# Performance work log

Measured on AMD Instinct MI355X. Metric: run time of the kernel, lower is better.

Reference implementation:

```python
import jax, jax.numpy as jnp
import numpy as np

SLOPE = 0.01  # LeakyReLU default negative slope
EPS = 1e-5    # BatchNorm eps


def _lrelu(x):
    return jnp.where(x >= 0, x, SLOPE * x)


def _conv(x, w, b):
    # x: [B,C,H,W], w: [O,I,kh,kw] (torch layout)
    y = jax.lax.conv_general_dilated(x, w, (1, 1), 'VALID',
                                     dimension_numbers=('NCHW', 'OIHW', 'NCHW'))
    return y + b[None, :, None, None]


def _bn4(x, p):
    # eval-mode BatchNorm2d; p = [gamma, beta, running_mean, running_var] stacked [4,C]
    g, b, m, v = p
    s = g * jax.lax.rsqrt(v + EPS)
    return x * s[None, :, None, None] + (b - m * s)[None, :, None, None]


def _forward(observation, action, sc1_w, sc1_b, sbn1, sc2_w, sc2_b, sbn2,
             mc1_w, mc1_b, mbn1, mc2_w, mc2_b, mbn2,
             gw_root, gw_rel, g_b, gbn,
             a_cw, a_cb, a_w1, a_b1, a_w2, a_b2, a_w3, a_b3,
             edge_index, edge_type, nodes_to_select):
    # ---- multi-scale temporal CNN (eval mode: dropout = identity) ----
    s = _lrelu(_bn4(_conv(observation, sc1_w, sc1_b), sbn1))
    s = _lrelu(_bn4(_conv(s, sc2_w, sc2_b), sbn2))          # [B,20,N,1]
    m = _lrelu(_bn4(_conv(observation, mc1_w, mc1_b), mbn1))
    m = _lrelu(_bn4(_conv(m, mc2_w, mc2_b), mbn2))          # [B,20,N,1]
    l = _lrelu(jnp.max(observation, axis=3, keepdims=True)) # [B,3,N,1]
    temporal = jnp.concatenate([s, m, l], axis=1)           # [B,43,N,1]

    # ---- RGCN (graph replicated per batch element; aggr='mean' per relation) ----
    x = jnp.swapaxes(temporal[..., 0], 1, 2)                # [B,N,F]
    N = x.shape[1]
    src, dst = edge_index[0], edge_index[1]
    out = jnp.einsum('bnf,fg->bng', x, gw_root) + g_b       # root transform + bias
    for r in range(gw_rel.shape[0]):
        h = jnp.einsum('bnf,fg->bng', x, gw_rel[r])         # per-relation transform
        mask = (edge_type == r).astype(x.dtype)             # [E]
        msgs = h[:, src, :] * mask[None, :, None]           # [B,E,F] gather
        agg = jax.ops.segment_sum(jnp.swapaxes(msgs, 0, 1), dst, num_segments=N)  # [N,B,F]
        deg = jax.ops.segment_sum(mask, dst, num_segments=N)                       # [N]
        out = out + jnp.swapaxes(agg, 0, 1) / jnp.maximum(deg, 1.0)[None, :, None]
    # BatchNorm1d (eval) + LeakyReLU; dropout = identity
    g, be, mu, v = gbn
    sg = g * jax.lax.rsqrt(v + EPS)
    out = _lrelu(out * sg + (be - mu * sg))                 # [B,N,F]

    graph_feats = jnp.swapaxes(out, 1, 2)[..., None]        # [B,F,N,1]
    feats = jnp.concatenate([temporal, graph_feats], axis=1)  # [B,86,N,1]
    feats = feats[:, :, nodes_to_select, :]                 # [B,86,P,1]

    # ---- actor head (mode == 'actor'); cash_bias is zeroed in the original ----
    stocks = action[:, 1:][:, None, :, None]                # [B,1,P,1]
    f = jnp.concatenate([stocks, feats], axis=1)[..., 0]    # [B,87,P]
    logits = jnp.einsum('bcp,c->bp', f, a_cw) + a_cb[0]     # 1x1 conv, out_ch=1
    o = jnp.concatenate([jnp.zeros((f.shape[0], 1), f.dtype), logits], axis=1)  # [B,P+1]
    h1 = jax.nn.relu(o @ a_w1 + a_b1)
    h2 = jax.nn.relu(h1 @ a_w2 + a_b2)
    return jax.nn.softmax(h2 @ a_w3 + a_b3, axis=-1)


def setup_inputs() -> dict:
    key = jax.random.key(0)
    ks = jax.random.split(key, 30)
    B, C0, N, T = 64, 3, 500, 50
    E, R, P, H = 16000, 4, 500, 128
    CM, CF = 3, 20
    F = 2 * CF + C0  # 43

    def rn(k, sh, s=0.1):
        return jax.random.normal(k, sh, jnp.float32) * s

    def bn_p(k, c):
        k1, k2, k3, k4 = jax.random.split(k, 4)
        return jnp.stack([jax.random.uniform(k1, (c,), jnp.float32, 0.5, 1.5),
                          rn(k2, (c,)), rn(k3, (c,)),
                          jax.random.uniform(k4, (c,), jnp.float32, 0.5, 1.5)])

    return {
        'observation': jax.random.normal(ks[0], (B, C0, N, T), jnp.float32),
        'action': jax.random.uniform(ks[1], (B, P + 1), jnp.float32),
        'edge_index': jax.random.randint(ks[2], (2, E), 0, N),
        'edge_type': jax.random.randint(ks[3], (E,), 0, R),
        'nodes_to_select': jnp.arange(P),
        'sc1_w': rn(ks[4], (CM, C0, 1, 3)), 'sc1_b': rn(ks[5], (CM,)), 'sbn1': bn_p(ks[6], CM),
        'sc2_w': rn(ks[7], (CF, CM, 1, 48)), 'sc2_b': rn(ks[8], (CF,)), 'sbn2': bn_p(ks[9], CF),
        'mc1_w': rn(ks[10], (CM, C0, 1, 21)), 'mc1_b': rn(ks[11], (CM,)), 'mbn1': bn_p(ks[12], CM),
        'mc2_w': rn(ks[13], (CF, CM, 1, 30)), 'mc2_b': rn(ks[14], (CF,)), 'mbn2': bn_p(ks[15], CF),
        'gw_root': rn(ks[16], (F, F)), 'gw_rel': rn(ks[17], (R, F, F)),
        'g_b': rn(ks[18], (F,)), 'gbn': bn_p(ks[19], F),
        'a_cw': rn(ks[20], (2 * F + 1,)), 'a_cb': rn(ks[21], (1,)),
        'a_w1': rn(ks[22], (P + 1, H)), 'a_b1': rn(ks[23], (H,)),
        'a_w2': rn(ks[24], (H, H)), 'a_b2': rn(ks[25], (H,)),
        'a_w3': rn(ks[26], (H, P + 1)), 'a_b3': rn(ks[27], (P + 1,)),
    }


def reference(observation, action, edge_index, edge_type, nodes_to_select,
              sc1_w, sc1_b, sbn1, sc2_w, sc2_b, sbn2,
              mc1_w, mc1_b, mbn1, mc2_w, mc2_b, mbn2,
              gw_root, gw_rel, g_b, gbn,
              a_cw, a_cb, a_w1, a_b1, a_w2, a_b2, a_w3, a_b3):
    return _forward(observation, action, sc1_w, sc1_b, sbn1, sc2_w, sc2_b, sbn2,
                    mc1_w, mc1_b, mbn1, mc2_w, mc2_b, mbn2,
                    gw_root, gw_rel, g_b, gbn,
                    a_cw, a_cb, a_w1, a_b1, a_w2, a_b2, a_w3, a_b3,
                    edge_index, edge_type, nodes_to_select)
```

## Files before the change

### kernel.cpp

```cpp
#include <hip/hip_runtime.h>

#define SLOPE 0.01f
#define EPSV  1e-5f
#define BB    64
#define NN    500
#define TT    50
#define E_N   16000
#define FF    43
#define PP    500
#define HH    128
#define XSTRIDE 48
#define PAD_E 40

typedef const float* fp;

__device__ __forceinline__ float lrelu(float x){ return x >= 0.f ? x : SLOPE * x; }
__device__ __forceinline__ float bnap(float x, fp bnp, int c, int C){
  float g  = bnp[c], b_ = bnp[C + c];
  float m  = bnp[2*C + c], v = bnp[3*C + c];
  float s = g * rsqrtf(v + EPSV);
  return x * s + (b_ - m * s);
}

__global__ __launch_bounds__(1024) void k_prep16(
    fp sc2w, fp mc2w, fp gwroot, fp gwrel,
    float* __restrict__ wT_s2, float* __restrict__ wT_m2, float* __restrict__ wTg,
    float* __restrict__ o_ws,
    const int* __restrict__ ei, const int* __restrict__ et,
    int* __restrict__ cntg, int* __restrict__ esp)
{
  int tid = threadIdx.x, blk = blockIdx.x;
  if (blk == 0){
    for (int i = tid; i < 2880; i += 1024){ int o = i/144, x = i%144; wT_s2[x*20+o] = sc2w[i]; }
  } else if (blk == 1){
    for (int i = tid; i < 1800; i += 1024){ int o = i/90,  x = i%90;  wT_m2[x*20+o] = mc2w[i]; }
  } else if (blk < 6){
    for (int i = (blk-2)*1024 + tid; i < 9245; i += 4096){
      int f5 = i/43, g = i%43;
      wTg[i] = (f5 < 43) ? gwroot[f5*43+g] : gwrel[(f5-43)*43+g];
    }
  } else if (blk == 6){
    if (tid < BB) o_ws[tid*(PP+1)] = 0.f;
  } else if (blk == 7){
    for (int i = 9245 + tid; i < 9312; i += 1024) wTg[i] = 0.f;
  } else {
    int e = (blk - 8)*1024 + tid;
    if (e < E_N){
      int s = ei[e], d = ei[E_N + e], r = et[e];
      int idx = d*4 + r;
      int pos = atomicAdd(&cntg[idx], 1);
      if (pos < PAD_E) esp[idx*PAD_E + pos] = s;
    }
  }
}

__global__ __launch_bounds__(512, 2) void k_tempo16(
    fp obs,
    fp sc1w, fp sc1b, fp sbn1, fp sc2b, fp sbn2,
    fp mc1w, fp mc1b, fp mbn1, fp mc2b, fp mbn2,
    const float* __restrict__ wT_s2, const float* __restrict__ wT_m2,
    float* __restrict__ xbuf)
{
  __shared__ float smem[11776];
  #define OL(n,j)   smem[(n)*151 + (j)]
  #define PB(w,n,o) smem[(w)*1472 + (n)*23 + (o)]
  int tid = threadIdx.x;

  int w = __builtin_amdgcn_readfirstlane(tid >> 6);
  int lane = tid & 63;
  int b  = blockIdx.x >> 3;
  int n0 = (blockIdx.x & 7) << 6;
  int span = (NN - n0 < 64) ? (NN - n0) : 64;

  for (int c = 0; c < 3; c++){
    const float* base = obs + (size_t)(b*3 + c)*25000;
    for (int idx = tid; idx < 3200; idx += 512){
      int n = idx / 50, t = idx % 50;
      int node = n0 + n; if (node > NN-1) node = NN-1;
      OL(n, c*50 + t) = base[node*50 + t];
    }
  }
  __syncthreads();

  float acc[20];
  float mx[3] = {-1e30f, -1e30f, -1e30f};
  if (w < 5){
    int t0 = w * 6;
    float ov[3][26];
    #pragma unroll
    for (int ci = 0; ci < 3; ci++)
      #pragma unroll
      for (int j = 0; j < 26; j++)
        ov[ci][j] = OL(lane, ci*50 + t0 + j);
    float sc1[3], sh1[3];
    #pragma unroll
    for (int ci = 0; ci < 3; ci++){
      float s = mbn1[ci] * rsqrtf(mbn1[9+ci] + EPSV);
      sc1[ci] = s; sh1[ci] = mbn1[3+ci] - mbn1[6+ci]*s;
    }
    #pragma unroll
    for (int o = 0; o < 20; o++) acc[o] = 0.f;
    #pragma unroll
    for (int i = 0; i < 6; i++){
      int tt = t0 + i;
      float mv[3];
      #pragma unroll
      for (int co = 0; co < 3; co++) mv[co] = mc1b[co];
      #pragma unroll
      for (int ci = 0; ci < 3; ci++)
        #pragma unroll
        for (int k = 0; k < 21; k++){
          float v = ov[ci][i + k];
          #pragma unroll
          for (int co = 0; co < 3; co++) mv[co] += v * mc1w[co*63 + ci*21 + k];
        }
      #pragma unroll
      for (int co = 0; co < 3; co++){
        float z = lrelu(mv[co]*sc1[co] + sh1[co]);
        const float* wp = wT_m2 + (co*30 + tt)*20;
        #pragma unroll
        for (int o = 0; o < 20; o++) acc[o] += z * wp[o];
      }
    }
  } else {
    int ws_ = w - 5;
    int t0 = ws_ * 16;
    float ovs[3][18];
    #pragma unroll
    for (int ci = 0; ci < 3; ci++)
      #pragma unroll
      for (int j = 0; j < 18; j++)
        ovs[ci][j] = OL(lane, ci*50 + t0 + j);
    int l0 = ws_ * 17;
    int ln = (50 - l0 < 17) ? (50 - l0) : 17;
    for (int j = 0; j < ln; j++){
      #pragma unroll
      for (int c = 0; c < 3; c++)
        mx[c] = fmaxf(mx[c], OL(lane, c*50 + l0 + j));
    }
    float sc1[3], sh1[3];
    #pragma unroll
    for (int ci = 0; ci < 3; ci++){
      float s = sbn1[ci] * rsqrtf(sbn1[9+ci] + EPSV);
      sc1[ci] = s; sh1[ci] = sbn1[3+ci] - sbn1[6+ci]*s;
    }
    #pragma unroll
    for (int o = 0; o < 20; o++) acc[o] = 0.f;
    #pragma unroll
    for (int i = 0; i < 16; i++){
      int tt = t0 + i;
      float sv[3];
      #pragma unroll
      for (int co = 0; co < 3; co++) sv[co] = sc1b[co];
      #pragma unroll
      for (int ci = 0; ci < 3; ci++)
        #pragma unroll
        for (int k = 0; k < 3; k++){
          float v = ovs[ci][i + k];
          #pragma unroll
          for (int co = 0; co < 3; co++) sv[co] += v * sc1w[co*9 + ci*3 + k];
        }
      #pragma unroll
      for (int co = 0; co < 3; co++){
        float z = lrelu(sv[co]*sc1[co] + sh1[co]);
        const float* wp = wT_s2 + (co*48 + tt)*20;
        #pragma unroll
        for (int o = 0; o < 20; o++) acc[o] += z * wp[o];
      }
    }
  }
  __syncthreads();

  #pragma unroll
  for (int o = 0; o < 20; o++) PB(w, lane, o) = acc[o];
  if (w >= 5){
    #pragma unroll
    for (int c = 0; c < 3; c++) PB(w, lane, 20 + c) = mx[c];
  }
  __syncthreads();

  size_t gx = (size_t)(b*NN + n0)*XSTRIDE;
  for (int idx = tid; idx < 64*20; idx += 512){
    int n = idx / 20, o = idx % 20;
    if (n < span){
      float v = PB(0,n,o) + PB(1,n,o) + PB(2,n,o) + PB(3,n,o) + PB(4,n,o);
      xbuf[gx + (size_t)n*XSTRIDE + 20 + o] = lrelu(bnap(v + mc2b[o], mbn2, o, 20));
    }
  }
  for (int idx = tid; idx < 64*20; idx += 512){
    int n = idx / 20, o = idx % 20;
    if (n < span){
      float v = PB(5,n,o) + PB(6,n,o) + PB(7,n,o);
      xbuf[gx + (size_t)n*XSTRIDE + o] = lrelu(bnap(v + sc2b[o], sbn2, o, 20));
    }
  }
  for (int idx = tid; idx < 64*3; idx += 512){
    int n = idx / 3, c = idx % 3;
    if (n < span){
      float v = fmaxf(fmaxf(PB(5,n,20+c), PB(6,n,20+c)), PB(7,n,20+c));
      xbuf[gx + (size_t)n*XSTRIDE + 40 + c] = lrelu(v);
    }
  }
  #undef OL
  #undef PB
}

__global__ __launch_bounds__(1024) void k_graph16(
    const float* __restrict__ xbuf, const float* __restrict__ wTg,
    fp gb, fp gbnp,
    const int* __restrict__ cntg, const int* __restrict__ esp,
    fp action, fp acw, fp acb,
    float* __restrict__ o_ws)
{
  __shared__ float xin[64][219];
  __shared__ float lred[16][64];
  int p = blockIdx.x;
  int l = ((p & 7) * 63) + (p >> 3);
  if (l >= 500) return;
  int tid = threadIdx.x;
  int w = tid >> 6, lane = tid & 63;
  int g0 = l * 64;

  for (int q = 0; q < 4; q++){
    int nl = (w << 2) + q;
    int g = __builtin_amdgcn_readfirstlane(g0 + nl);
    int b = g / NN;
    int n = g - b * NN;
    const float* xb = xbuf + (size_t)(b * NN) * XSTRIDE;
    float xv = (lane < FF) ? xbuf[(size_t)g*XSTRIDE + lane] : 0.f;
    float ar[4];
    #pragma unroll
    for (int r = 0; r < 4; r++){
      int idx = n*4 + r;
      int c = __builtin_amdgcn_readfirstlane(cntg[idx]);
      if (c > PAD_E) c = PAD_E;
      const int* ep = esp + idx*PAD_E;
      float a0 = 0.f, a1 = 0.f, a2 = 0.f, a3 = 0.f;
      int i = 0;
      for (; i + 4 <= c; i += 4){
        int s0 = ep[i], s1 = ep[i+1], s2 = ep[i+2], s3 = ep[i+3];
        float v0 = (lane < FF) ? xb[(size_t)s0*XSTRIDE + lane] : 0.f;
        float v1 = (lane < FF) ? xb[(size_t)s1*XSTRIDE + lane] : 0.f;
        float v2 = (lane < FF) ? xb[(size_t)s2*XSTRIDE + lane] : 0.f;
        float v3 = (lane < FF) ? xb[(size_t)s3*XSTRIDE + lane] : 0.f;
        a0 += v0; a1 += v1; a2 += v2; a3 += v3;
      }
      for (; i < c; i++){
        int s = ep[i];
        a0 += (lane < FF) ? xb[(size_t)s*XSTRIDE + lane] : 0.f;
      }
      ar[r] = ((a0 + a1) + (a2 + a3)) / fmaxf((float)c, 1.f);
    }
    if (lane < FF){
      xin[nl][lane]       = xv;
      xin[nl][ 43 + lane] = ar[0];
      xin[nl][ 86 + lane] = ar[1];
      xin[nl][129 + lane] = ar[2];
      xin[nl][172 + lane] = ar[3];
    }
  }
  __syncthreads();

  int c0 = __builtin_amdgcn_readfirstlane(w * 3);
  float acc[3];
  #pragma unroll
  for (int j = 0; j < 3; j++) acc[j] = (c0 + j < FF) ? gb[c0+j] : 0.f;
  for (int f = 0; f < 215; f++){
    float v = xin[lane][f];
    const float* wp = wTg + f*43 + c0;
    #pragma unroll
    for (int j = 0; j < 3; j++) acc[j] += v * wp[j];
  }
  float lp = 0.f;
  #pragma unroll
  for (int j = 0; j < 3; j++){
    int c = c0 + j;
    if (c < FF){
      float gv = lrelu(bnap(acc[j], gbnp, c, FF));
      lp += gv * acw[1 + FF + c];
    }
  }
  if (w == 15){
    int g = g0 + lane;
    int b = g / NN, n = g - b * NN;
    float xp = acb[0] + action[b*(PP+1) + 1 + n] * acw[0];
    #pragma unroll 2
    for (int c = 0; c < FF; c++) xp += xin[lane][c] * acw[1 + c];
    lp = xp;
  }
  lred[w][lane] = lp;
  __syncthreads();
  if (tid < 64){
    float t = 0.f;
    #pragma unroll
    for (int w2 = 0; w2 < 16; w2++) t += lred[w2][tid];
    int g2 = g0 + tid;
    int b = g2 / NN, n = g2 - b * NN;
    o_ws[b*(PP+1) + 1 + n] = t;
  }
}

__global__ __launch_bounds__(512) void k_fcall(
    const float* __restrict__ o_ws,
    fp aw1, fp ab1, fp aw2, fp ab2, fp aw3, fp ab3,
    float* __restrict__ out)
{
  int b = blockIdx.x;
  int tid = threadIdx.x;
  __shared__ float os[PP+1];
  __shared__ float part[4][HH];
  __shared__ float h1[HH];
  __shared__ float h2[HH];
  __shared__ float red[512];

  if (tid <= PP) os[tid] = o_ws[b*(PP+1) + tid];
  __syncthreads();

  {
    int chunk = tid >> 7, h = tid & 127;
    int k0 = chunk * 125;
    int kn = (chunk == 3) ? 126 : 125;
    float acc = 0.f;
    for (int k = 0; k < kn; k++) acc += os[k0+k] * aw1[(k0+k)*HH + h];
    part[chunk][h] = acc;
  }
  __syncthreads();
  if (tid < HH)
    h1[tid] = fmaxf(ab1[tid] + part[0][tid] + part[1][tid] + part[2][tid] + part[3][tid], 0.f);
  __syncthreads();
  if (tid < HH){
    float acc = ab2[tid];
    #pragma unroll 4
    for (int k = 0; k < HH; k++) acc += h1[k] * aw2[k*HH + tid];
    h2[tid] = fmaxf(acc, 0.f);
  }
  __syncthreads();

  float val = -1e30f;
  if (tid <= PP){
    float acc = ab3[tid];
    #pragma unroll 4
    for (int k = 0; k < HH; k++) acc += h2[k] * aw3[k*(PP+1) + tid];
    val = acc;
  }
  red[tid] = val;
  __syncthreads();
  for (int s = 256; s > 0; s >>= 1){
    if (tid < s) red[tid] = fmaxf(red[tid], red[tid + s]);
    __syncthreads();
  }
  float mxv = red[0];
  __syncthreads();
  float e = (tid <= PP) ? expf(val - mxv) : 0.f;
  red[tid] = e;
  __syncthreads();
  for (int s = 256; s > 0; s >>= 1){
    if (tid < s) red[tid] += red[tid + s];
    __syncthreads();
  }
  float sum = red[0];
  if (tid <= PP) out[b*(PP+1) + tid] = e / sum;
}

extern "C" void kernel_launch(void* const* d_in, const int* in_sizes, int n_in,
                              void* d_out, int out_size, void* d_ws, size_t ws_size,
                              hipStream_t stream)
{
  fp obs    = (fp)d_in[0];
  fp action = (fp)d_in[1];
  const int* ei  = (const int*)d_in[2];
  const int* et  = (const int*)d_in[3];
  fp sc1w=(fp)d_in[5],  sc1b=(fp)d_in[6],  sbn1=(fp)d_in[7];
  fp sc2w=(fp)d_in[8],  sc2b=(fp)d_in[9],  sbn2=(fp)d_in[10];
  fp mc1w=(fp)d_in[11], mc1b=(fp)d_in[12], mbn1=(fp)d_in[13];
  fp mc2w=(fp)d_in[14], mc2b=(fp)d_in[15], mbn2=(fp)d_in[16];
  fp gwroot=(fp)d_in[17], gwrel=(fp)d_in[18], gb=(fp)d_in[19], gbnp=(fp)d_in[20];
  fp acw=(fp)d_in[21], acb=(fp)d_in[22];
  fp aw1=(fp)d_in[23], ab1=(fp)d_in[24];
  fp aw2=(fp)d_in[25], ab2=(fp)d_in[26];
  fp aw3=(fp)d_in[27], ab3=(fp)d_in[28];

  float* xbuf   = (float*)d_ws;
  float* wT_s2  = xbuf + 1536000;
  float* wT_m2  = wT_s2 + 2880;
  float* wTg    = wT_m2 + 1800;
  float* o_ws   = wTg + 9312;
  int*   cntg   = (int*)(o_ws + 32064);
  int*   esp    = cntg + 2000;

  float* out = (float*)d_out;

  hipMemsetAsync(cntg, 0, 2000*sizeof(int), stream);
  hipLaunchKernelGGL(k_prep16, dim3(24), dim3(1024), 0, stream,
    sc2w, mc2w, gwroot, gwrel, wT_s2, wT_m2, wTg, o_ws, ei, et, cntg, esp);
  hipLaunchKernelGGL(k_tempo16, dim3(512), dim3(512), 0, stream,
    obs, sc1w, sc1b, sbn1, sc2b, sbn2,
    mc1w, mc1b, mbn1, mc2b, mbn2, wT_s2, wT_m2, xbuf);
  hipLaunchKernelGGL(k_graph16, dim3(504), dim3(1024), 0, stream,
    xbuf, wTg, gb, gbnp, cntg, esp, action, acw, acb, o_ws);
  hipLaunchKernelGGL(k_fcall, dim3(BB), dim3(512), 0, stream,
    o_ws, aw1, ab1, aw2, ab2, aw3, ab3, out);
}
```

Before: 248.8 us.

## Restructure temporal CNN kernel to 16 lanes per node with DPP reductions

Result: slower. 476.7 us (+91.6%).

```diff
diff --git a/kernel.cpp b/kernel.cpp
--- a/kernel.cpp
+++ b/kernel.cpp
@@ -22,10 +22,28 @@
   return x * s + (b_ - m * s);
 }
 
-__global__ __launch_bounds__(1024) void k_prep16(
+#define DPP_I(x, c) __builtin_amdgcn_update_dpp(0, (x), (c), 0xF, 0xF, true)
+__device__ __forceinline__ float rsum16(float x){
+  x += __int_as_float(DPP_I(__float_as_int(x), 0xB1));
+  x += __int_as_float(DPP_I(__float_as_int(x), 0x4E));
+  x += __int_as_float(DPP_I(__float_as_int(x), 0x124));
+  x += __int_as_float(DPP_I(__float_as_int(x), 0x128));
+  return x;
+}
+__device__ __forceinline__ float rmax16(float x){
+  x = fmaxf(x, __int_as_float(DPP_I(__float_as_int(x), 0xB1)));
+  x = fmaxf(x, __int_as_float(DPP_I(__float_as_int(x), 0x4E)));
+  x = fmaxf(x, __int_as_float(DPP_I(__float_as_int(x), 0x124)));
+  x = fmaxf(x, __int_as_float(DPP_I(__float_as_int(x), 0x128)));
+  return x;
+}
+
+__global__ __launch_bounds__(1024) void k_prep17(
     fp sc2w, fp mc2w, fp gwroot, fp gwrel,
+    fp sc1b, fp sbn1, fp mc1b, fp mbn1,
+    fp sc2b, fp sbn2, fp mc2b, fp mbn2,
     float* __restrict__ wT_s2, float* __restrict__ wT_m2, float* __restrict__ wTg,
-    float* __restrict__ o_ws,
+    float* __restrict__ tbl, float* __restrict__ o_ws,
     const int* __restrict__ ei, const int* __restrict__ et,
     int* __restrict__ cntg, int* __restrict__ esp)
 {
@@ -41,6 +59,28 @@
     }
   } else if (blk == 6){
     if (tid < BB) o_ws[tid*(PP+1)] = 0.f;
+    if (tid < 20){
+      float g = sbn2[tid], b_ = sbn2[20+tid], m = sbn2[40+tid], v = sbn2[60+tid];
+      float s = g * rsqrtf(v + EPSV);
+      tbl[tid] = s; tbl[43+tid] = sc2b[tid]*s + (b_ - m*s);
+    } else if (tid < 40){
+      int o = tid - 20;
+      float g = mbn2[o], b_ = mbn2[20+o], m = mbn2[40+o], v = mbn2[60+o];
+      float s = g * rsqrtf(v + EPSV);
+      tbl[tid] = s; tbl[43+tid] = mc2b[o]*s + (b_ - m*s);
+    } else if (tid < 43){
+      tbl[tid] = 1.f; tbl[43+tid] = 0.f;
+    } else if (tid < 46){
+      int ci = tid - 43;
+      float g = sbn1[ci], b_ = sbn1[3+ci], m = sbn1[6+ci], v = sbn1[9+ci];
+      float s = g * rsqrtf(v + EPSV);
+      tbl[86+ci] = s; tbl[89+ci] = sc1b[ci]*s + (b_ - m*s);
+    } else if (tid < 49){
+      int ci = tid - 46;
+      float g = mbn1[ci], b_ = mbn1[3+ci], m = mbn1[6+ci], v = mbn1[9+ci];
+      float s = g * rsqrtf(v + EPSV);
+      tbl[92+ci] = s; tbl[95+ci] = mc1b[ci]*s + (b_ - m*s);
+    }
   } else if (blk == 7){
     for (int i = 9245 + tid; i < 9312; i += 1024) wTg[i] = 0.f;
   } else {
@@ -54,155 +94,147 @@
   }
 }
 
-__global__ __launch_bounds__(512, 2) void k_tempo16(
-    fp obs,
-    fp sc1w, fp sc1b, fp sbn1, fp sc2b, fp sbn2,
-    fp mc1w, fp mc1b, fp mbn1, fp mc2b, fp mbn2,
+__global__ __launch_bounds__(128, 6) void k_tempo17(
+    fp obs, fp sc1w, fp mc1w,
     const float* __restrict__ wT_s2, const float* __restrict__ wT_m2,
+    const float* __restrict__ tbl,
     float* __restrict__ xbuf)
 {
-  __shared__ float smem[11776];
-  #define OL(n,j)   smem[(n)*151 + (j)]
-  #define PB(w,n,o) smem[(w)*1472 + (n)*23 + (o)]
-  int tid = threadIdx.x;
-
-  int w = __builtin_amdgcn_readfirstlane(tid >> 6);
-  int lane = tid & 63;
-  int b  = blockIdx.x >> 3;
-  int n0 = (blockIdx.x & 7) << 6;
-  int span = (NN - n0 < 64) ? (NN - n0) : 64;
+  __shared__ float OL[1288];
+  int tid  = threadIdx.x;
+  int w    = tid >> 6, lane = tid & 63;
+  int node = lane >> 4, seg = lane & 15;
+  int gg   = __builtin_amdgcn_readfirstlane(blockIdx.x*2 + w);
+  int b    = gg / 125, ng = gg - b*125;
+  int n0   = ng * 4;
+  int wbase = w * 612;
 
   for (int c = 0; c < 3; c++){
-    const float* base = obs + (size_t)(b*3 + c)*25000;
-    for (int idx = tid; idx < 3200; idx += 512){
-      int n = idx / 50, t = idx % 50;
-      int node = n0 + n; if (node > NN-1) node = NN-1;
-      OL(n, c*50 + t) = base[node*50 + t];
-    }
-  }
-  __syncthreads();
-
+    if (lane < 50){
+      const float4 v = *(const float4*)(obs + ((size_t)(b*3+c)*NN + n0)*TT + lane*4);
+      int f = lane*4;
+      int n = f/50, t = f - n*50;
+      int a = wbase + c*204 + n*51 + t;
+      OL[a] = v.x;
+      if (++t == 50){ t = 0; n++; a = wbase + c*204 + n*51; } else a++;
+      OL[a] = v.y;
+      if (++t == 50){ t = 0; n++; a = wbase + c*204 + n*51; } else a++;
+      OL[a] = v.z;
+      if (++t == 50){ t = 0; n++; a = wbase + c*204 + n*51; } else a++;
+      OL[a] = v.w;
+    }
+  }
+  __syncthreads();
+
+  int rb = wbase + node*51;
+  int g  = b*NN + n0 + node;
+  float* xr = xbuf + (size_t)g * XSTRIDE;
   float acc[20];
-  float mx[3] = {-1e30f, -1e30f, -1e30f};
-  if (w < 5){
-    int t0 = w * 6;
-    float ov[3][26];
-    #pragma unroll
-    for (int ci = 0; ci < 3; ci++)
+
+  {
+    float mv[3][3];
+    #pragma unroll
+    for (int i = 0; i < 3; i++)
       #pragma unroll
-      for (int j = 0; j < 26; j++)
-        ov[ci][j] = OL(lane, ci*50 + t0 + j);
-    float sc1[3], sh1[3];
+      for (int co = 0; co < 3; co++) mv[i][co] = 0.f;
+    int t0 = seg*3;
     #pragma unroll
     for (int ci = 0; ci < 3; ci++){
-      float s = mbn1[ci] * rsqrtf(mbn1[9+ci] + EPSV);
-      sc1[ci] = s; sh1[ci] = mbn1[3+ci] - mbn1[6+ci]*s;
-    }
-    #pragma unroll
-    for (int o = 0; o < 20; o++) acc[o] = 0.f;
-    #pragma unroll
-    for (int i = 0; i < 6; i++){
-      int tt = t0 + i;
-      float mv[3];
-      #pragma unroll
-      for (int co = 0; co < 3; co++) mv[co] = mc1b[co];
-      #pragma unroll
-      for (int ci = 0; ci < 3; ci++)
-        #pragma unroll
-        for (int k = 0; k < 21; k++){
-          float v = ov[ci][i + k];
-          #pragma unroll
-          for (int co = 0; co < 3; co++) mv[co] += v * mc1w[co*63 + ci*21 + k];
-        }
+      int ab = rb + ci*204 + t0;
+      float v0 = OL[ab], v1 = OL[ab+1], v2 = OL[ab+2], v3 = OL[ab+3], v4 = OL[ab+4];
       #pragma unroll
       for (int co = 0; co < 3; co++){
-        float z = lrelu(mv[co]*sc1[co] + sh1[co]);
-        const float* wp = wT_m2 + (co*30 + tt)*20;
-        #pragma unroll
-        for (int o = 0; o < 20; o++) acc[o] += z * wp[o];
-      }
-    }
-  } else {
-    int ws_ = w - 5;
-    int t0 = ws_ * 16;
-    float ovs[3][18];
-    #pragma unroll
-    for (int ci = 0; ci < 3; ci++)
-      #pragma unroll
-      for (int j = 0; j < 18; j++)
-        ovs[ci][j] = OL(lane, ci*50 + t0 + j);
-    int l0 = ws_ * 17;
-    int ln = (50 - l0 < 17) ? (50 - l0) : 17;
-    for (int j = 0; j < ln; j++){
-      #pragma unroll
-      for (int c = 0; c < 3; c++)
-        mx[c] = fmaxf(mx[c], OL(lane, c*50 + l0 + j));
-    }
-    float sc1[3], sh1[3];
-    #pragma unroll
-    for (int ci = 0; ci < 3; ci++){
-      float s = sbn1[ci] * rsqrtf(sbn1[9+ci] + EPSV);
-      sc1[ci] = s; sh1[ci] = sbn1[3+ci] - sbn1[6+ci]*s;
+        float w0 = sc1w[co*9+ci*3+0], w1 = sc1w[co*9+ci*3+1], w2 = sc1w[co*9+ci*3+2];
+        mv[0][co] += v0*w0 + v1*w1 + v2*w2;
+        mv[1][co] += v1*w0 + v2*w1 + v3*w2;
+        mv[2][co] += v2*w0 + v3*w1 + v4*w2;
+      }
     }
     #pragma unroll
     for (int o = 0; o < 20; o++) acc[o] = 0.f;
     #pragma unroll
-    for (int i = 0; i < 16; i++){
+    for (int i = 0; i < 3; i++){
       int tt = t0 + i;
-      float sv[3];
-      #pragma unroll
-      for (int co = 0; co < 3; co++) sv[co] = sc1b[co];
-      #pragma unroll
-      for (int ci = 0; ci < 3; ci++)
-        #pragma unroll
-        for (int k = 0; k < 3; k++){
-          float v = ovs[ci][i + k];
-          #pragma unroll
-          for (int co = 0; co < 3; co++) sv[co] += v * sc1w[co*9 + ci*3 + k];
-        }
       #pragma unroll
       for (int co = 0; co < 3; co++){
-        float z = lrelu(sv[co]*sc1[co] + sh1[co]);
-        const float* wp = wT_s2 + (co*48 + tt)*20;
+        float z = lrelu(mv[i][co]*tbl[86+co] + tbl[89+co]);
+        const float* wr = wT_s2 + (co*48+tt)*20;
         #pragma unroll
-        for (int o = 0; o < 20; o++) acc[o] += z * wp[o];
-      }
-    }
-  }
-  __syncthreads();
-
-  #pragma unroll
-  for (int o = 0; o < 20; o++) PB(w, lane, o) = acc[o];
-  if (w >= 5){
-    #pragma unroll
-    for (int c = 0; c < 3; c++) PB(w, lane, 20 + c) = mx[c];
-  }
-  __syncthreads();
-
-  size_t gx = (size_t)(b*NN + n0)*XSTRIDE;
-  for (int idx = tid; idx < 64*20; idx += 512){
-    int n = idx / 20, o = idx % 20;
-    if (n < span){
-      float v = PB(0,n,o) + PB(1,n,o) + PB(2,n,o) + PB(3,n,o) + PB(4,n,o);
-      xbuf[gx + (size_t)n*XSTRIDE + 20 + o] = lrelu(bnap(v + mc2b[o], mbn2, o, 20));
-    }
-  }
-  for (int idx = tid; idx < 64*20; idx += 512){
-    int n = idx / 20, o = idx % 20;
-    if (n < span){
-      float v = PB(5,n,o) + PB(6,n,o) + PB(7,n,o);
-      xbuf[gx + (size_t)n*XSTRIDE + o] = lrelu(bnap(v + sc2b[o], sbn2, o, 20));
-    }
-  }
-  for (int idx = tid; idx < 64*3; idx += 512){
-    int n = idx / 3, c = idx % 3;
-    if (n < span){
-      float v = fmaxf(fmaxf(PB(5,n,20+c), PB(6,n,20+c)), PB(7,n,20+c));
-      xbuf[gx + (size_t)n*XSTRIDE + 40 + c] = lrelu(v);
-    }
-  }
-  #undef OL
-  #undef PB
+        for (int o = 0; o < 20; o += 4){
+          float4 q = *(const float4*)(wr + o);
+          acc[o]+=z*q.x; acc[o+1]+=z*q.y; acc[o+2]+=z*q.z; acc[o+3]+=z*q.w;
+        }
+      }
+    }
+    #pragma unroll
+    for (int o = 0; o < 20; o++) acc[o] = rsum16(acc[o]);
+    #pragma unroll
+    for (int o = 0; o < 20; o++)
+      if (seg == (o & 15)) xr[o] = lrelu(acc[o]*tbl[o] + tbl[43+o]);
+  }
+
+  {
+    float mv[2][3];
+    #pragma unroll
+    for (int i = 0; i < 2; i++)
+      #pragma unroll
+      for (int co = 0; co < 3; co++) mv[i][co] = 0.f;
+    int t0 = seg*2;
+    #pragma unroll
+    for (int ci = 0; ci < 3; ci++){
+      int ab = rb + ci*204 + t0;
+      float vc = OL[ab];
+      #pragma unroll
+      for (int k = 0; k < 21; k++){
+        float vn = OL[ab + k + 1];
+        #pragma unroll
+        for (int co = 0; co < 3; co++){
+          float wk = mc1w[co*63 + ci*21 + k];
+          mv[0][co] += vc*wk;
+          mv[1][co] += vn*wk;
+        }
+        vc = vn;
+      }
+    }
+    #pragma unroll
+    for (int o = 0; o < 20; o++) acc[o] = 0.f;
+    #pragma unroll
+    for (int i = 0; i < 2; i++){
+      int tt = t0 + i;
+      if (tt < 30){
+        #pragma unroll
+        for (int co = 0; co < 3; co++){
+          float z = lrelu(mv[i][co]*tbl[92+co] + tbl[95+co]);
+          const float* wr = wT_m2 + (co*30+tt)*20;
+          #pragma unroll
+          for (int o = 0; o < 20; o += 4){
+            float4 q = *(const float4*)(wr + o);
+            acc[o]+=z*q.x; acc[o+1]+=z*q.y; acc[o+2]+=z*q.z; acc[o+3]+=z*q.w;
+          }
+        }
+      }
+    }
+    #pragma unroll
+    for (int o = 0; o < 20; o++) acc[o] = rsum16(acc[o]);
+    #pragma unroll
+    for (int o = 0; o < 20; o++)
+      if (seg == (o & 15)) xr[20+o] = lrelu(acc[o]*tbl[20+o] + tbl[63+o]);
+  }
+
+  {
+    float m0 = -3e38f, m1 = -3e38f, m2 = -3e38f;
+    int l0 = seg*4;
+    int ln = 50 - l0; if (ln > 4) ln = 4;
+    for (int j = 0; j < ln; j++){
+      m0 = fmaxf(m0, OL[rb +       l0 + j]);
+      m1 = fmaxf(m1, OL[rb + 204 + l0 + j]);
+      m2 = fmaxf(m2, OL[rb + 408 + l0 + j]);
+    }
+    m0 = rmax16(m0); m1 = rmax16(m1); m2 = rmax16(m2);
+    if (seg == 0) xr[40] = lrelu(m0);
+    if (seg == 1) xr[41] = lrelu(m1);
+    if (seg == 2) xr[42] = lrelu(m2);
+  }
 }
 
 __global__ __launch_bounds__(1024) void k_graph16(
@@ -384,18 +416,20 @@
   float* wT_s2  = xbuf + 1536000;
   float* wT_m2  = wT_s2 + 2880;
   float* wTg    = wT_m2 + 1800;
-  float* o_ws   = wTg + 9312;
+  float* tbl    = wTg + 9312;
+  float* o_ws   = tbl + 128;
   int*   cntg   = (int*)(o_ws + 32064);
   int*   esp    = cntg + 2000;
 
   float* out = (float*)d_out;
 
   hipMemsetAsync(cntg, 0, 2000*sizeof(int), stream);
-  hipLaunchKernelGGL(k_prep16, dim3(24), dim3(1024), 0, stream,
-    sc2w, mc2w, gwroot, gwrel, wT_s2, wT_m2, wTg, o_ws, ei, et, cntg, esp);
-  hipLaunchKernelGGL(k_tempo16, dim3(512), dim3(512), 0, stream,
-    obs, sc1w, sc1b, sbn1, sc2b, sbn2,
-    mc1w, mc1b, mbn1, mc2b, mbn2, wT_s2, wT_m2, xbuf);
+  hipLaunchKernelGGL(k_prep17, dim3(24), dim3(1024), 0, stream,
+    sc2w, mc2w, gwroot, gwrel,
+    sc1b, sbn1, mc1b, mbn1, sc2b, sbn2, mc2b, mbn2,
+    wT_s2, wT_m2, wTg, tbl, o_ws, ei, et, cntg, esp);
+  hipLaunchKernelGGL(k_tempo17, dim3(4000), dim3(128), 0, stream,
+    obs, sc1w, mc1w, wT_s2, wT_m2, tbl, xbuf);
   hipLaunchKernelGGL(k_graph16, dim3(504), dim3(1024), 0, stream,
     xbuf, wTg, gb, gbnp, cntg, esp, action, acw, acb, o_ws);
   hipLaunchKernelGGL(k_fcall, dim3(BB), dim3(512), 0, stream,
```
